# Performance work log

Measured on AMD Instinct MI355X. Metric: run time of the kernel, lower is better.

## Reference

```python
import jax, jax.numpy as jnp
import numpy as np

N_ATOMS = 10000
N_EDGES = 320000
F = 128
LN_EPS = 1e-5
VN_EPS = 1e-8


def _layer_norm(x, gamma, beta):
    mu = jnp.mean(x, axis=-1, keepdims=True)
    var = jnp.mean(jnp.square(x - mu), axis=-1, keepdims=True)
    return (x - mu) * jax.lax.rsqrt(var + LN_EPS) * gamma + beta


def _vector_norm(x):
    # Equivariant RMS normalization: per-channel vector norms, RMS over channels.
    sq = jnp.sum(jnp.square(x), axis=1, keepdims=True)          # [N,1,F]
    rms = jnp.sqrt(jnp.mean(sq, axis=-1, keepdims=True) + VN_EPS)  # [N,1,1]
    return x / rms


def setup_inputs() -> dict:
    key = jax.random.key(0)
    ks = jax.random.split(key, 16)
    rn = lambda k, shape, s=1.0: jax.random.normal(k, shape, dtype=jnp.float32) * s
    w_s = 0.05  # small init scale for weights
    return {
        "h": rn(ks[0], (N_ATOMS, 1, F)),
        "v": rn(ks[1], (N_ATOMS, 3, F)),
        "H": rn(ks[2], (N_ATOMS, 1, F)),
        "V": rn(ks[3], (N_ATOMS, 3, F)),
        "Wij": rn(ks[4], (N_EDGES, 1, 3 * F)),
        "dir_ij": rn(ks[5], (N_EDGES, 3)),
        "W1": rn(ks[6], (F, F), w_s),
        "b1": jnp.zeros((F,), jnp.float32),
        "W2": rn(ks[7], (F, 3 * F), w_s),
        "b2": jnp.zeros((3 * F,), jnp.float32),
        "Wmix": rn(ks[8], (F, 2 * F), w_s),
        "Wh_remain": rn(ks[9], (F, F), w_s),
        "Wh_forget": rn(ks[10], (F, F), w_s),
        "Wv_remain": rn(ks[11], (F, 1), w_s),
        "gamma": jnp.ones((F,), jnp.float32),
        "beta": jnp.zeros((F,), jnp.float32),
        "idx_i": jnp.sort(jax.random.randint(ks[12], (N_EDGES,), 0, N_ATOMS)),
        "idx_j": jax.random.randint(ks[13], (N_EDGES,), 0, N_ATOMS),
        "n_atoms": N_ATOMS,
    }


def reference(h, v, H, V, Wij, dir_ij, W1, b1, W2, b2, Wmix,
              Wh_remain, Wh_forget, Wv_remain, gamma, beta,
              idx_i, idx_j, n_atoms):
    # interatomic context net: Dense(F,F,silu) -> Dense(F,3F)
    X = jax.nn.silu(H @ W1 + b1) @ W2 + b2            # [N,1,3F]
    Hj = X[idx_j]                                      # [E,1,3F]
    Vj = V[idx_j]                                      # [E,3,F]
    Xe = Wij * Hj                                      # [E,1,3F]
    dh_e, dvR, dvv = jnp.split(Xe, 3, axis=-1)         # each [E,1,F]
    dh = jax.ops.segment_sum(dh_e, idx_i, num_segments=n_atoms)  # [N,1,F]
    dv_e = dvR * dir_ij[:, :, None] + dvv * Vj         # [E,3,F]
    dv = jax.ops.segment_sum(dv_e, idx_i, num_segments=n_atoms)  # [N,3,F]

    v_mix = v @ Wmix                                   # [N,3,2F]
    v_V, v_W = jnp.split(v_mix, 2, axis=-1)
    ctx = jnp.sum(v_V * v_W, axis=1, keepdims=True)    # [N,1,F]

    q = _layer_norm(h + dh @ Wh_remain + (dh @ Wh_forget) * ctx, gamma, beta)
    mu = _vector_norm(v + dv + (dh @ Wv_remain) * v)
    return q, mu
```

## Files before the change

kernel.cpp:

```cpp
#include <hip/hip_runtime.h>
#include <math.h>

#define FDIM 128
#define F3   384

static constexpr int K1_R = 8;
static constexpr int K2_R = 8;
static constexpr int K4_R = 4;
static constexpr int CHUNK = 64;

typedef float vf4 __attribute__((ext_vector_type(4)));

__device__ __forceinline__ vf4 fma4(vf4 a, vf4 b, vf4 c) {
    vf4 r;
    r[0] = fmaf(a[0], b[0], c[0]);
    r[1] = fmaf(a[1], b[1], c[1]);
    r[2] = fmaf(a[2], b[2], c[2]);
    r[3] = fmaf(a[3], b[3], c[3]);
    return r;
}
__device__ __forceinline__ vf4 fma4s(vf4 a, float s, vf4 c) {
    vf4 r;
    r[0] = fmaf(a[0], s, c[0]);
    r[1] = fmaf(a[1], s, c[1]);
    r[2] = fmaf(a[2], s, c[2]);
    r[3] = fmaf(a[3], s, c[3]);
    return r;
}

__global__ __launch_bounds__(256) void k0_seg(
    const int* __restrict__ idx_i, int* __restrict__ seg, int E, int N)
{
    int n = blockIdx.x * 256 + threadIdx.x;
    if (n > N) return;
    if (n == N) { seg[n] = E; return; }
    int lo = 0, hi = E;
    while (lo < hi) {
        int m = (lo + hi) >> 1;
        if (idx_i[m] < n) lo = m + 1; else hi = m;
    }
    seg[n] = lo;
}

__global__ __launch_bounds__(128) void k1_ctxnet(
    const float* __restrict__ H,  const float* __restrict__ W1,
    const float* __restrict__ b1, const float* __restrict__ W2,
    const float* __restrict__ b2, float* __restrict__ X, int N)
{
    __shared__ float sH[K1_R][FDIM];
    __shared__ float sT[K1_R][FDIM];
    const int f  = threadIdx.x;
    const int n0 = blockIdx.x * K1_R;

    for (int r = 0; r < K1_R; ++r) {
        int n = n0 + r;
        sH[r][f] = (n < N) ? H[(size_t)n * FDIM + f] : 0.f;
    }
    __syncthreads();

    float acc[K1_R];
    #pragma unroll
    for (int r = 0; r < K1_R; ++r) acc[r] = 0.f;
    #pragma unroll 4
    for (int a = 0; a < FDIM; ++a) {
        float w = W1[a * FDIM + f];
        #pragma unroll
        for (int r = 0; r < K1_R; ++r) acc[r] = fmaf(sH[r][a], w, acc[r]);
    }
    float bb = b1[f];
    #pragma unroll
    for (int r = 0; r < K1_R; ++r) {
        float t = acc[r] + bb;
        sT[r][f] = t / (1.f + expf(-t));
    }
    __syncthreads();

    float a0[K1_R], a1[K1_R], a2[K1_R];
    #pragma unroll
    for (int r = 0; r < K1_R; ++r) { a0[r] = 0.f; a1[r] = 0.f; a2[r] = 0.f; }
    #pragma unroll 4
    for (int a = 0; a < FDIM; ++a) {
        float w0 = W2[a * F3 + f];
        float w1 = W2[a * F3 + FDIM + f];
        float w2 = W2[a * F3 + 2 * FDIM + f];
        #pragma unroll
        for (int r = 0; r < K1_R; ++r) {
            float t = sT[r][a];
            a0[r] = fmaf(t, w0, a0[r]);
            a1[r] = fmaf(t, w1, a1[r]);
            a2[r] = fmaf(t, w2, a2[r]);
        }
    }
    float c0 = b2[f], c1 = b2[FDIM + f], c2 = b2[2 * FDIM + f];
    for (int r = 0; r < K1_R; ++r) {
        int n = n0 + r;
        if (n < N) {
            X[(size_t)n * F3 + f]            = a0[r] + c0;
            X[(size_t)n * F3 + FDIM + f]     = a1[r] + c1;
            X[(size_t)n * F3 + 2 * FDIM + f] = a2[r] + c2;
        }
    }
}

__global__ __launch_bounds__(128) void k2_ctx(
    const float* __restrict__ v, const float* __restrict__ Wmix,
    float* __restrict__ ctx, int N)
{
    __shared__ float sv[3][K2_R][FDIM];
    const int f  = threadIdx.x;
    const int n0 = blockIdx.x * K2_R;

    for (int r = 0; r < K2_R; ++r) {
        int n = n0 + r;
        for (int d = 0; d < 3; ++d)
            sv[d][r][f] = (n < N) ? v[((size_t)n * 3 + d) * FDIM + f] : 0.f;
    }
    __syncthreads();

    float cacc[K2_R];
    #pragma unroll
    for (int r = 0; r < K2_R; ++r) cacc[r] = 0.f;

    for (int d = 0; d < 3; ++d) {
        float aV[K2_R], aW[K2_R];
        #pragma unroll
        for (int r = 0; r < K2_R; ++r) { aV[r] = 0.f; aW[r] = 0.f; }
        #pragma unroll 4
        for (int a = 0; a < FDIM; ++a) {
            float w0 = Wmix[a * (2 * FDIM) + f];
            float w1 = Wmix[a * (2 * FDIM) + FDIM + f];
            #pragma unroll
            for (int r = 0; r < K2_R; ++r) {
                float t = sv[d][r][a];
                aV[r] = fmaf(t, w0, aV[r]);
                aW[r] = fmaf(t, w1, aW[r]);
            }
        }
        #pragma unroll
        for (int r = 0; r < K2_R; ++r) cacc[r] = fmaf(aV[r], aW[r], cacc[r]);
    }
    for (int r = 0; r < K2_R; ++r) {
        int n = n0 + r;
        if (n < N) ctx[(size_t)n * FDIM + f] = cacc[r];
    }
}

__global__ __launch_bounds__(256) void k3_edges(
    const float* __restrict__ X, const float* __restrict__ V,
    const float* __restrict__ Wij, const float* __restrict__ dir_ij,
    const int* __restrict__ seg, const int* __restrict__ idx_j,
    float* __restrict__ dh, float* __restrict__ dv)
{
    const int n   = blockIdx.x;
    const int tid = threadIdx.x;
    const int g   = tid >> 5;
    const int l   = tid & 31;

    __shared__ int   sj[CHUNK];
    __shared__ float sd[CHUNK][4];
    __shared__ vf4   sacc[8][4][32];

    const int e0 = seg[n];
    const int e1 = seg[n + 1];

    vf4 adh = {0.f, 0.f, 0.f, 0.f};
    vf4 a0  = {0.f, 0.f, 0.f, 0.f};
    vf4 a1  = {0.f, 0.f, 0.f, 0.f};
    vf4 a2  = {0.f, 0.f, 0.f, 0.f};

    for (int base = e0; base < e1; base += CHUNK) {
        const int cnt = (e1 - base < CHUNK) ? (e1 - base) : CHUNK;
        if (tid < cnt) sj[tid] = idx_j[base + tid];
        for (int t = tid; t < 3 * cnt; t += 256)
            sd[t / 3][t % 3] = dir_ij[(size_t)base * 3 + t];
        __syncthreads();

        int kk = g;
        for (; kk + 8 < cnt; kk += 16) {
            const int eA = base + kk,     jA = sj[kk];
            const int eB = base + kk + 8, jB = sj[kk + 8];
            const vf4* wA = (const vf4*)(Wij + (size_t)eA * F3);
            const vf4* xA = (const vf4*)(X   + (size_t)jA * F3);
            const vf4* qA = (const vf4*)(V   + (size_t)jA * F3);
            const vf4* wB = (const vf4*)(Wij + (size_t)eB * F3);
            const vf4* xB = (const vf4*)(X   + (size_t)jB * F3);
            const vf4* qB = (const vf4*)(V   + (size_t)jB * F3);

            vf4 wA0 = __builtin_nontemporal_load(wA + l);
            vf4 wA1 = __builtin_nontemporal_load(wA + 32 + l);
            vf4 wA2 = __builtin_nontemporal_load(wA + 64 + l);
            vf4 xA0 = xA[l], xA1 = xA[32 + l], xA2 = xA[64 + l];
            vf4 vA0 = qA[l], vA1 = qA[32 + l], vA2 = qA[64 + l];
            vf4 wB0 = __builtin_nontemporal_load(wB + l);
            vf4 wB1 = __builtin_nontemporal_load(wB + 32 + l);
            vf4 wB2 = __builtin_nontemporal_load(wB + 64 + l);
            vf4 xB0 = xB[l], xB1 = xB[32 + l], xB2 = xB[64 + l];
            vf4 vB0 = qB[l], vB1 = qB[32 + l], vB2 = qB[64 + l];

            const float dA0 = sd[kk][0],     dA1 = sd[kk][1],     dA2 = sd[kk][2];
            const float dB0 = sd[kk + 8][0], dB1 = sd[kk + 8][1], dB2 = sd[kk + 8][2];

            adh = fma4(wA0, xA0, adh);
            {
                vf4 r = wA1 * xA1, s = wA2 * xA2;
                a0 = fma4s(r, dA0, fma4(s, vA0, a0));
                a1 = fma4s(r, dA1, fma4(s, vA1, a1));
                a2 = fma4s(r, dA2, fma4(s, vA2, a2));
            }
            adh = fma4(wB0, xB0, adh);
            {
                vf4 r = wB1 * xB1, s = wB2 * xB2;
                a0 = fma4s(r, dB0, fma4(s, vB0, a0));
                a1 = fma4s(r, dB1, fma4(s, vB1, a1));
                a2 = fma4s(r, dB2, fma4(s, vB2, a2));
            }
        }
        for (; kk < cnt; kk += 8) {
            const int e = base + kk, j = sj[kk];
            const vf4* w = (const vf4*)(Wij + (size_t)e * F3);
            const vf4* x = (const vf4*)(X   + (size_t)j * F3);
            const vf4* q = (const vf4*)(V   + (size_t)j * F3);
            vf4 w0 = __builtin_nontemporal_load(w + l);
            vf4 w1 = __builtin_nontemporal_load(w + 32 + l);
            vf4 w2 = __builtin_nontemporal_load(w + 64 + l);
            vf4 x0 = x[l], x1 = x[32 + l], x2 = x[64 + l];
            vf4 v0 = q[l], v1 = q[32 + l], v2 = q[64 + l];
            const float d0 = sd[kk][0], d1 = sd[kk][1], d2 = sd[kk][2];

            adh = fma4(w0, x0, adh);
            vf4 r = w1 * x1, s = w2 * x2;
            a0 = fma4s(r, d0, fma4(s, v0, a0));
            a1 = fma4s(r, d1, fma4(s, v1, a1));
            a2 = fma4s(r, d2, fma4(s, v2, a2));
        }
        __syncthreads();
    }

    sacc[g][0][l] = adh;
    sacc[g][1][l] = a0;
    sacc[g][2][l] = a1;
    sacc[g][3][l] = a2;
    __syncthreads();

    if (tid < 128) {
        const int c  = tid >> 5;
        const int ll = tid & 31;
        vf4 s = sacc[0][c][ll];
        #pragma unroll
        for (int gg = 1; gg < 8; ++gg) s += sacc[gg][c][ll];
        if (c == 0)
            ((vf4*)(dh + (size_t)n * FDIM))[ll] = s;
        else
            ((vf4*)(dv + (size_t)n * F3))[(c - 1) * 32 + ll] = s;
    }
}

__device__ inline float block_reduce_sum_128(float val, float* tmp) {
    #pragma unroll
    for (int o = 32; o > 0; o >>= 1) val += __shfl_down(val, o, 64);
    const int tid = threadIdx.x;
    if ((tid & 63) == 0) tmp[tid >> 6] = val;
    __syncthreads();
    float r = tmp[0] + tmp[1];
    __syncthreads();
    return r;
}

__global__ __launch_bounds__(128) void k4_epilogue(
    const float* __restrict__ h,   const float* __restrict__ v,
    const float* __restrict__ dh,  const float* __restrict__ dv,
    const float* __restrict__ ctx,
    const float* __restrict__ Whr, const float* __restrict__ Whf,
    const float* __restrict__ Wvr,
    const float* __restrict__ gamma, const float* __restrict__ beta,
    float* __restrict__ q, float* __restrict__ mu, int N)
{
    __shared__ float sdh[K4_R][FDIM];
    __shared__ float sred[2];
    const int f  = threadIdx.x;
    const int n0 = blockIdx.x * K4_R;

    for (int r = 0; r < K4_R; ++r) {
        int n = n0 + r;
        sdh[r][f] = (n < N) ? dh[(size_t)n * FDIM + f] : 0.f;
    }
    __syncthreads();

    float accR[K4_R], accF[K4_R];
    #pragma unroll
    for (int r = 0; r < K4_R; ++r) { accR[r] = 0.f; accF[r] = 0.f; }
    #pragma unroll 4
    for (int a = 0; a < FDIM; ++a) {
        float wr = Whr[a * FDIM + f];
        float wf = Whf[a * FDIM + f];
        #pragma unroll
        for (int r = 0; r < K4_R; ++r) {
            accR[r] = fmaf(sdh[r][a], wr, accR[r]);
            accF[r] = fmaf(sdh[r][a], wf, accF[r]);
        }
    }

    const float wv = Wvr[f];
    const float g  = gamma[f];
    const float bt = beta[f];

    for (int r = 0; r < K4_R; ++r) {
        int n = n0 + r;
        if (n >= N) break;

        float s = block_reduce_sum_128(sdh[r][f] * wv, sred);

        float u    = h[(size_t)n * FDIM + f] + accR[r] + accF[r] * ctx[(size_t)n * FDIM + f];
        float mean = block_reduce_sum_128(u, sred) * (1.f / 128.f);
        float dlt  = u - mean;
        float var  = block_reduce_sum_128(dlt * dlt, sred) * (1.f / 128.f);
        q[(size_t)n * FDIM + f] = dlt * rsqrtf(var + 1e-5f) * g + bt;

        float sc = 1.f + s;
        float x0 = fmaf(v[((size_t)n * 3 + 0) * FDIM + f], sc, dv[(size_t)n * F3 + f]);
        float x1 = fmaf(v[((size_t)n * 3 + 1) * FDIM + f], sc, dv[(size_t)n * F3 + FDIM + f]);
        float x2 = fmaf(v[((size_t)n * 3 + 2) * FDIM + f], sc, dv[(size_t)n * F3 + 2 * FDIM + f]);
        float sq  = x0 * x0 + x1 * x1 + x2 * x2;
        float tot = block_reduce_sum_128(sq, sred) * (1.f / 128.f);
        float inv = rsqrtf(tot + 1e-8f);
        mu[((size_t)n * 3 + 0) * FDIM + f] = x0 * inv;
        mu[((size_t)n * 3 + 1) * FDIM + f] = x1 * inv;
        mu[((size_t)n * 3 + 2) * FDIM + f] = x2 * inv;
    }
}

extern "C" void kernel_launch(void* const* d_in, const int* in_sizes, int n_in,
                              void* d_out, int out_size, void* d_ws, size_t ws_size,
                              hipStream_t stream)
{
    const float* h     = (const float*)d_in[0];
    const float* v     = (const float*)d_in[1];
    const float* H     = (const float*)d_in[2];
    const float* V     = (const float*)d_in[3];
    const float* Wij   = (const float*)d_in[4];
    const float* dir   = (const float*)d_in[5];
    const float* W1    = (const float*)d_in[6];
    const float* b1    = (const float*)d_in[7];
    const float* W2    = (const float*)d_in[8];
    const float* b2    = (const float*)d_in[9];
    const float* Wmix  = (const float*)d_in[10];
    const float* Whr   = (const float*)d_in[11];
    const float* Whf   = (const float*)d_in[12];
    const float* Wvr   = (const float*)d_in[13];
    const float* gamma = (const float*)d_in[14];
    const float* beta  = (const float*)d_in[15];
    const int*   idx_i = (const int*)d_in[16];
    const int*   idx_j = (const int*)d_in[17];

    const int N = in_sizes[0] / FDIM;
    const int E = in_sizes[16];

    float* ws  = (float*)d_ws;
    float* X   = ws;
    float* ctx = X   + (size_t)N * F3;
    float* dh  = ctx + (size_t)N * FDIM;
    float* dv  = dh  + (size_t)N * FDIM;
    int*   seg = (int*)(dv + (size_t)N * F3);

    float* q   = (float*)d_out;
    float* mu  = q + (size_t)N * FDIM;

    hipLaunchKernelGGL(k0_seg, dim3((N + 256) / 256), dim3(256), 0, stream,
                       idx_i, seg, E, N);
    hipLaunchKernelGGL(k1_ctxnet, dim3((N + K1_R - 1) / K1_R), dim3(128), 0, stream,
                       H, W1, b1, W2, b2, X, N);
    hipLaunchKernelGGL(k2_ctx, dim3((N + K2_R - 1) / K2_R), dim3(128), 0, stream,
                       v, Wmix, ctx, N);
    hipLaunchKernelGGL(k3_edges, dim3(N), dim3(256), 0, stream,
                       X, V, Wij, dir, seg, idx_j, dh, dv);
    hipLaunchKernelGGL(k4_epilogue, dim3((N + K4_R - 1) / K4_R), dim3(128), 0, stream,
                       h, v, dh, dv, ctx, Whr, Whf, Wvr, gamma, beta, q, mu, N);
}
```

Measured before the change: 888.3 us.

## Fuse context-net and vector-mix kernels, pair epilogue reductions, reorder edge loads

Merges the context MLP kernel and the Wmix/ctx kernel into one launch that shares a block over the same atom rows. In the epilogue, four block reductions become two paired reductions, which cuts the number of barriers per row. In the edge kernel, the gathered X/V loads are issued before the streaming Wij loads so the random gathers start earlier. The fused kernel uses more shared memory and registers, which may lower its occupancy.

```diff
diff --git a/kernel.cpp b/kernel.cpp
--- a/kernel.cpp
+++ b/kernel.cpp
@@ -5,7 +5,6 @@
 #define F3   384
 
 static constexpr int K1_R = 8;
-static constexpr int K2_R = 8;
 static constexpr int K4_R = 4;
 static constexpr int CHUNK = 64;
 
@@ -42,19 +41,24 @@
     seg[n] = lo;
 }
 
-__global__ __launch_bounds__(128) void k1_ctxnet(
+__global__ __launch_bounds__(128) void k12_ctxnet_mix(
     const float* __restrict__ H,  const float* __restrict__ W1,
     const float* __restrict__ b1, const float* __restrict__ W2,
-    const float* __restrict__ b2, float* __restrict__ X, int N)
+    const float* __restrict__ b2,
+    const float* __restrict__ v,  const float* __restrict__ Wmix,
+    float* __restrict__ X, float* __restrict__ ctx, int N)
 {
     __shared__ float sH[K1_R][FDIM];
     __shared__ float sT[K1_R][FDIM];
+    __shared__ float sv[3][K1_R][FDIM];
     const int f  = threadIdx.x;
     const int n0 = blockIdx.x * K1_R;
 
     for (int r = 0; r < K1_R; ++r) {
         int n = n0 + r;
         sH[r][f] = (n < N) ? H[(size_t)n * FDIM + f] : 0.f;
+        for (int d = 0; d < 3; ++d)
+            sv[d][r][f] = (n < N) ? v[((size_t)n * 3 + d) * FDIM + f] : 0.f;
     }
     __syncthreads();
 
@@ -100,46 +104,29 @@
             X[(size_t)n * F3 + 2 * FDIM + f] = a2[r] + c2;
         }
     }
-}
-
-__global__ __launch_bounds__(128) void k2_ctx(
-    const float* __restrict__ v, const float* __restrict__ Wmix,
-    float* __restrict__ ctx, int N)
-{
-    __shared__ float sv[3][K2_R][FDIM];
-    const int f  = threadIdx.x;
-    const int n0 = blockIdx.x * K2_R;
-
-    for (int r = 0; r < K2_R; ++r) {
-        int n = n0 + r;
-        for (int d = 0; d < 3; ++d)
-            sv[d][r][f] = (n < N) ? v[((size_t)n * 3 + d) * FDIM + f] : 0.f;
-    }
-    __syncthreads();
-
-    float cacc[K2_R];
-    #pragma unroll
-    for (int r = 0; r < K2_R; ++r) cacc[r] = 0.f;
-
+
+    float cacc[K1_R];
+    #pragma unroll
+    for (int r = 0; r < K1_R; ++r) cacc[r] = 0.f;
     for (int d = 0; d < 3; ++d) {
-        float aV[K2_R], aW[K2_R];
-        #pragma unroll
-        for (int r = 0; r < K2_R; ++r) { aV[r] = 0.f; aW[r] = 0.f; }
+        float aV[K1_R], aW[K1_R];
+        #pragma unroll
+        for (int r = 0; r < K1_R; ++r) { aV[r] = 0.f; aW[r] = 0.f; }
         #pragma unroll 4
         for (int a = 0; a < FDIM; ++a) {
             float w0 = Wmix[a * (2 * FDIM) + f];
             float w1 = Wmix[a * (2 * FDIM) + FDIM + f];
             #pragma unroll
-            for (int r = 0; r < K2_R; ++r) {
+            for (int r = 0; r < K1_R; ++r) {
                 float t = sv[d][r][a];
                 aV[r] = fmaf(t, w0, aV[r]);
                 aW[r] = fmaf(t, w1, aW[r]);
             }
         }
         #pragma unroll
-        for (int r = 0; r < K2_R; ++r) cacc[r] = fmaf(aV[r], aW[r], cacc[r]);
-    }
-    for (int r = 0; r < K2_R; ++r) {
+        for (int r = 0; r < K1_R; ++r) cacc[r] = fmaf(aV[r], aW[r], cacc[r]);
+    }
+    for (int r = 0; r < K1_R; ++r) {
         int n = n0 + r;
         if (n < N) ctx[(size_t)n * FDIM + f] = cacc[r];
     }
@@ -186,16 +173,16 @@
             const vf4* xB = (const vf4*)(X   + (size_t)jB * F3);
             const vf4* qB = (const vf4*)(V   + (size_t)jB * F3);
 
+            vf4 xA0 = xA[l], xA1 = xA[32 + l], xA2 = xA[64 + l];
+            vf4 vA0 = qA[l], vA1 = qA[32 + l], vA2 = qA[64 + l];
+            vf4 xB0 = xB[l], xB1 = xB[32 + l], xB2 = xB[64 + l];
+            vf4 vB0 = qB[l], vB1 = qB[32 + l], vB2 = qB[64 + l];
             vf4 wA0 = __builtin_nontemporal_load(wA + l);
             vf4 wA1 = __builtin_nontemporal_load(wA + 32 + l);
             vf4 wA2 = __builtin_nontemporal_load(wA + 64 + l);
-            vf4 xA0 = xA[l], xA1 = xA[32 + l], xA2 = xA[64 + l];
-            vf4 vA0 = qA[l], vA1 = qA[32 + l], vA2 = qA[64 + l];
             vf4 wB0 = __builtin_nontemporal_load(wB + l);
             vf4 wB1 = __builtin_nontemporal_load(wB + 32 + l);
             vf4 wB2 = __builtin_nontemporal_load(wB + 64 + l);
-            vf4 xB0 = xB[l], xB1 = xB[32 + l], xB2 = xB[64 + l];
-            vf4 vB0 = qB[l], vB1 = qB[32 + l], vB2 = qB[64 + l];
 
             const float dA0 = sd[kk][0],     dA1 = sd[kk][1],     dA2 = sd[kk][2];
             const float dB0 = sd[kk + 8][0], dB1 = sd[kk + 8][1], dB2 = sd[kk + 8][2];
@@ -220,11 +207,11 @@
             const vf4* w = (const vf4*)(Wij + (size_t)e * F3);
             const vf4* x = (const vf4*)(X   + (size_t)j * F3);
             const vf4* q = (const vf4*)(V   + (size_t)j * F3);
+            vf4 x0 = x[l], x1 = x[32 + l], x2 = x[64 + l];
+            vf4 v0 = q[l], v1 = q[32 + l], v2 = q[64 + l];
             vf4 w0 = __builtin_nontemporal_load(w + l);
             vf4 w1 = __builtin_nontemporal_load(w + 32 + l);
             vf4 w2 = __builtin_nontemporal_load(w + 64 + l);
-            vf4 x0 = x[l], x1 = x[32 + l], x2 = x[64 + l];
-            vf4 v0 = q[l], v1 = q[32 + l], v2 = q[64 + l];
             const float d0 = sd[kk][0], d1 = sd[kk][1], d2 = sd[kk][2];
 
             adh = fma4(w0, x0, adh);
@@ -255,15 +242,21 @@
     }
 }
 
-__device__ inline float block_reduce_sum_128(float val, float* tmp) {
-    #pragma unroll
-    for (int o = 32; o > 0; o >>= 1) val += __shfl_down(val, o, 64);
+__device__ __forceinline__ void block_reduce2_128(float& a, float& b, float* tmp) {
+    #pragma unroll
+    for (int o = 32; o > 0; o >>= 1) {
+        a += __shfl_down(a, o, 64);
+        b += __shfl_down(b, o, 64);
+    }
     const int tid = threadIdx.x;
-    if ((tid & 63) == 0) tmp[tid >> 6] = val;
-    __syncthreads();
-    float r = tmp[0] + tmp[1];
-    __syncthreads();
-    return r;
+    if ((tid & 63) == 0) {
+        tmp[(tid >> 6) * 2]     = a;
+        tmp[(tid >> 6) * 2 + 1] = b;
+    }
+    __syncthreads();
+    a = tmp[0] + tmp[2];
+    b = tmp[1] + tmp[3];
+    __syncthreads();
 }
 
 __global__ __launch_bounds__(128) void k4_epilogue(
@@ -276,7 +269,7 @@
     float* __restrict__ q, float* __restrict__ mu, int N)
 {
     __shared__ float sdh[K4_R][FDIM];
-    __shared__ float sred[2];
+    __shared__ float sred[4];
     const int f  = threadIdx.x;
     const int n0 = blockIdx.x * K4_R;
 
@@ -308,21 +301,26 @@
         int n = n0 + r;
         if (n >= N) break;
 
-        float s = block_reduce_sum_128(sdh[r][f] * wv, sred);
-
-        float u    = h[(size_t)n * FDIM + f] + accR[r] + accF[r] * ctx[(size_t)n * FDIM + f];
-        float mean = block_reduce_sum_128(u, sred) * (1.f / 128.f);
+        float u  = h[(size_t)n * FDIM + f] + accR[r]
+                 + accF[r] * ctx[(size_t)n * FDIM + f];
+        float su = u;
+        float s  = sdh[r][f] * wv;
+        block_reduce2_128(su, s, sred);
+
+        float mean = su * (1.f / 128.f);
         float dlt  = u - mean;
-        float var  = block_reduce_sum_128(dlt * dlt, sred) * (1.f / 128.f);
-        q[(size_t)n * FDIM + f] = dlt * rsqrtf(var + 1e-5f) * g + bt;
-
-        float sc = 1.f + s;
+        float sc   = 1.f + s;
         float x0 = fmaf(v[((size_t)n * 3 + 0) * FDIM + f], sc, dv[(size_t)n * F3 + f]);
         float x1 = fmaf(v[((size_t)n * 3 + 1) * FDIM + f], sc, dv[(size_t)n * F3 + FDIM + f]);
         float x2 = fmaf(v[((size_t)n * 3 + 2) * FDIM + f], sc, dv[(size_t)n * F3 + 2 * FDIM + f]);
+
+        float var = dlt * dlt;
         float sq  = x0 * x0 + x1 * x1 + x2 * x2;
-        float tot = block_reduce_sum_128(sq, sred) * (1.f / 128.f);
-        float inv = rsqrtf(tot + 1e-8f);
+        block_reduce2_128(var, sq, sred);
+
+        q[(size_t)n * FDIM + f] = dlt * rsqrtf(var * (1.f / 128.f) + 1e-5f) * g + bt;
+
+        float inv = rsqrtf(sq * (1.f / 128.f) + 1e-8f);
         mu[((size_t)n * 3 + 0) * FDIM + f] = x0 * inv;
         mu[((size_t)n * 3 + 1) * FDIM + f] = x1 * inv;
         mu[((size_t)n * 3 + 2) * FDIM + f] = x2 * inv;
@@ -367,10 +365,8 @@
 
     hipLaunchKernelGGL(k0_seg, dim3((N + 256) / 256), dim3(256), 0, stream,
                        idx_i, seg, E, N);
-    hipLaunchKernelGGL(k1_ctxnet, dim3((N + K1_R - 1) / K1_R), dim3(128), 0, stream,
-                       H, W1, b1, W2, b2, X, N);
-    hipLaunchKernelGGL(k2_ctx, dim3((N + K2_R - 1) / K2_R), dim3(128), 0, stream,
-                       v, Wmix, ctx, N);
+    hipLaunchKernelGGL(k12_ctxnet_mix, dim3((N + K1_R - 1) / K1_R), dim3(128), 0, stream,
+                       H, W1, b1, W2, b2, v, Wmix, X, ctx, N);
     hipLaunchKernelGGL(k3_edges, dim3(N), dim3(256), 0, stream,
                        X, V, Wij, dir, seg, idx_j, dh, dv);
     hipLaunchKernelGGL(k4_epilogue, dim3((N + K4_R - 1) / K4_R), dim3(128), 0, stream,
```

Result: no change. 886.9 us (-0.2%).
